# Performance work log

Hardware: AMD Instinct MI355X
Metric: run time of the kernel (lower is better)

## Reference

```python
import jax, jax.numpy as jnp
import numpy as np

B, T, C, H = 4, 1024, 512, 8
HD = C // H
N_NODE, F_DIM, TOTAL_DIM = 64, 8, 16
SCALE = 1.0 / np.sqrt(HD)


def _build_mask():
    # causal tril with every (total_dim-1 mod total_dim)-th COLUMN zeroed
    m = np.tril(np.ones((T, T), dtype=np.float32))
    m[:, TOTAL_DIM - 1::TOTAL_DIM] = 0.0
    return jnp.asarray(m)

MASK = _build_mask()  # (T, T), 1 = keep, 0 = mask


def setup_inputs() -> dict:
    key = jax.random.key(0)
    ks = jax.random.split(key, 12)
    s = 0.02
    return {
        "x": jax.random.normal(ks[0], (B, T, C), dtype=jnp.float32),
        "attn_bias": jax.random.normal(ks[1], (H, N_NODE, N_NODE), dtype=jnp.float32) * 0.1,
        "Wq": jax.random.normal(ks[2], (C, C), dtype=jnp.float32) * s,
        "bq": jax.random.normal(ks[3], (C,), dtype=jnp.float32) * s,
        "Wk": jax.random.normal(ks[4], (C, C), dtype=jnp.float32) * s,
        "bk": jax.random.normal(ks[5], (C,), dtype=jnp.float32) * s,
        "Wv": jax.random.normal(ks[6], (C, C), dtype=jnp.float32) * s,
        "bv": jax.random.normal(ks[7], (C,), dtype=jnp.float32) * s,
        "Wp": jax.random.normal(ks[8], (C, C), dtype=jnp.float32) * s,
        "bp": jax.random.normal(ks[9], (C,), dtype=jnp.float32) * s,
    }


def reference(x, attn_bias, Wq, bq, Wk, bk, Wv, bv, Wp, bp):
    Bx, Tx, Cx = x.shape

    def heads(W, b):  # (B,T,C) -> (B,H,T,HD); torch Linear is x @ W.T + b
        return (x @ W.T + b).reshape(Bx, Tx, H, HD).transpose(0, 2, 1, 3)

    q, k, v = heads(Wq, bq), heads(Wk, bk), heads(Wv, bv)

    # repeat_interleave + repeat expansion == kron(attn_bias, ones(f_dim, f_dim))
    d = N_NODE * F_DIM
    bias = jnp.repeat(jnp.repeat(attn_bias, F_DIM, axis=1), F_DIM, axis=2)  # (H, d, d)
    padded_bias = jnp.zeros((H, Tx, Tx), dtype=x.dtype).at[:, :d, :d].set(bias)

    att = jnp.einsum('bhqd,bhkd->bhqk', q, k) * SCALE + padded_bias[None]
    neg = jnp.asarray(-jnp.inf, dtype=att.dtype)
    att = jnp.where(MASK[None, None, :Tx, :Tx] == 0, neg, att)
    att = jax.nn.softmax(att, axis=-1)

    y = jnp.einsum('bhqk,bhkd->bhqd', att, v)
    y = y.transpose(0, 2, 1, 3).reshape(Bx, Tx, Cx)
    return y @ Wp.T + bp
```

## Files before the change

kernel.cpp:

```cpp
#include <hip/hip_runtime.h>

#define T_SEQ 1024
#define C_DIM 512
#define H_HEADS 8
#define HDIM 64
#define B_BATCH 4
#define M_ROWS (B_BATCH * T_SEQ)
#define NSPLIT_TOT 40

typedef __attribute__((ext_vector_type(8))) short short8;
typedef __attribute__((ext_vector_type(4))) float f32x4;

__device__ __forceinline__ unsigned short f2bf(float f) {
    unsigned u = __builtin_bit_cast(unsigned, f);
    u += 0x7FFFu + ((u >> 16) & 1u);
    return (unsigned short)(u >> 16);
}

__device__ __forceinline__ float bf2f(unsigned short u) {
    return __builtin_bit_cast(float, (unsigned)u << 16);
}

__device__ __forceinline__ void gload_lds16(const unsigned short* g, unsigned short* l) {
    __builtin_amdgcn_global_load_lds(
        (const __attribute__((address_space(1))) unsigned int*)(const void*)g,
        (__attribute__((address_space(3))) unsigned int*)(void*)l, 16, 0, 0);
}

__device__ __constant__ unsigned char BX_OF[NSPLIT_TOT] =
    {0,1,2,3,4,4,5,5,6,6,7,7,8,8,8,9,9,9,10,10,10,11,11,11,
     12,12,12,12,13,13,13,13,14,14,14,14,15,15,15,15};
__device__ __constant__ unsigned char SP_OF[NSPLIT_TOT] =
    {0,0,0,0,0,1,0,1,0,1,0,1,0,1,2,0,1,2,0,1,2,0,1,2,
     0,1,2,3,0,1,2,3,0,1,2,3,0,1,2,3};
__device__ __constant__ unsigned char CUM_OF[16] =
    {0,1,2,3,4,6,8,10,12,15,18,21,24,28,32,36};

__global__ __launch_bounds__(256) void cast_all(
    const float* __restrict__ x,
    const float* __restrict__ wq, const float* __restrict__ wk,
    const float* __restrict__ wv, const float* __restrict__ wp,
    unsigned short* __restrict__ xb,
    unsigned short* __restrict__ wqb, unsigned short* __restrict__ wkb,
    unsigned short* __restrict__ wvb, unsigned short* __restrict__ wpb)
{
    const long NX = (long)M_ROWS * C_DIM;
    const long NW = (long)C_DIM * C_DIM;
    long i4 = (long)blockIdx.x * blockDim.x + threadIdx.x;
    long base = i4 * 4;
    const float* src; unsigned short* dst; long off;
    if (base < NX) { src = x; dst = xb; off = base; }
    else {
        long r = base - NX;
        int w = (int)(r >> 18);
        off = r & (NW - 1);
        switch (w) {
            case 0:  src = wq; dst = wqb; break;
            case 1:  src = wk; dst = wkb; break;
            case 2:  src = wv; dst = wvb; break;
            default: src = wp; dst = wpb; break;
        }
    }
    float4 v = *(const float4*)(src + off);
    ushort4 o;
    o.x = f2bf(v.x); o.y = f2bf(v.y); o.z = f2bf(v.z); o.w = f2bf(v.w);
    *(ushort4*)(dst + off) = o;
}

__device__ __forceinline__ void gemm_body(
    const unsigned short* __restrict__ A,
    const unsigned short* __restrict__ W,
    const float* __restrict__ bias,
    unsigned short* __restrict__ Obf,
    float* __restrict__ Of,
    int mode)
{
    __shared__ __align__(16) unsigned short Atile[128 * 64];
    __shared__ __align__(16) unsigned short Btile[64 * 64];

    const int tid  = threadIdx.x;
    const int w    = tid >> 6;
    const int lane = tid & 63;
    const int quad = lane >> 4;
    const int l16  = lane & 15;
    const int m0   = blockIdx.x * 128;
    const int n0   = blockIdx.y * 64;

    f32x4 acc[2][4] = {};

    const int lr = lane >> 3;
    const int lc = lane & 7;

    for (int k0 = 0; k0 < 512; k0 += 64) {
        __syncthreads();
        for (int i = 0; i < 4; ++i) {
            int r0 = 32 * w + 8 * i;
            int r  = r0 + lr;
            int c  = lc ^ (r & 7);
            gload_lds16(&A[(long)(m0 + r) * 512 + k0 + c * 8], &Atile[r0 * 64]);
        }
        for (int i = 0; i < 2; ++i) {
            int r0 = 16 * w + 8 * i;
            int r  = r0 + lr;
            int c  = lc ^ (r & 7);
            gload_lds16(&W[(long)(n0 + r) * 512 + k0 + c * 8], &Btile[r0 * 64]);
        }
        __syncthreads();

        for (int st = 0; st < 2; ++st) {
            const int pc = ((4 * st + quad) ^ (l16 & 7)) * 8;
            short8 af[2], bf[4];
            for (int i = 0; i < 2; ++i)
                af[i] = *(const short8*)&Atile[(32 * w + 16 * i + l16) * 64 + pc];
            for (int j = 0; j < 4; ++j)
                bf[j] = *(const short8*)&Btile[(16 * j + l16) * 64 + pc];
            for (int i = 0; i < 2; ++i)
                for (int j = 0; j < 4; ++j)
                    acc[i][j] = (mode == 1)
                        ? __builtin_amdgcn_mfma_f32_16x16x32_bf16(bf[j], af[i], acc[i][j], 0, 0, 0)
                        : __builtin_amdgcn_mfma_f32_16x16x32_bf16(af[i], bf[j], acc[i][j], 0, 0, 0);
        }
    }

    if (mode == 1) {
        for (int j = 0; j < 4; ++j) {
            for (int reg = 0; reg < 4; ++reg) {
                int n = n0 + 16 * j + 4 * quad + reg;
                int h = n >> 6, hd = n & 63;
                float bv = bias[n];
                for (int i = 0; i < 2; ++i) {
                    int t = m0 + 32 * w + 16 * i + l16;
                    int b = t >> 10, tl = t & 1023;
                    Obf[(((long)(b * H_HEADS + h)) * HDIM + hd) * T_SEQ + tl] =
                        f2bf(acc[i][j][reg] + bv);
                }
            }
        }
    } else {
        for (int j = 0; j < 4; ++j) {
            int col = n0 + 16 * j + l16;
            float bv = bias[col];
            for (int i = 0; i < 2; ++i) {
                for (int reg = 0; reg < 4; ++reg) {
                    int row = m0 + 32 * w + 16 * i + 4 * quad + reg;
                    float v = acc[i][j][reg] + bv;
                    if (mode == 2) {
                        Of[(long)row * 512 + col] = v;
                    } else {
                        int b = row >> 10, t = row & 1023;
                        int h = col >> 6,  hd = col & 63;
                        Obf[(((long)(b * H_HEADS + h)) * T_SEQ + t) * HDIM + hd] = f2bf(v);
                    }
                }
            }
        }
    }
}

__global__ __launch_bounds__(256) void gemm_qkv(
    const unsigned short* __restrict__ A,
    const unsigned short* __restrict__ Wq, const unsigned short* __restrict__ Wk,
    const unsigned short* __restrict__ Wv,
    const float* __restrict__ bq, const float* __restrict__ bk, const float* __restrict__ bv,
    unsigned short* __restrict__ Q, unsigned short* __restrict__ K,
    unsigned short* __restrict__ V)
{
    const unsigned short* W; const float* b; unsigned short* O; int mode;
    if (blockIdx.z == 0)      { W = Wq; b = bq; O = Q; mode = 0; }
    else if (blockIdx.z == 1) { W = Wk; b = bk; O = K; mode = 0; }
    else                      { W = Wv; b = bv; O = V; mode = 1; }
    gemm_body(A, W, b, O, nullptr, mode);
}

__global__ __launch_bounds__(256) void gemm_out_k(
    const unsigned short* __restrict__ A, const unsigned short* __restrict__ W,
    const float* __restrict__ bias, float* __restrict__ O)
{
    gemm_body(A, W, bias, nullptr, O, 2);
}

__global__ __launch_bounds__(256) void attn_split(
    const unsigned short* __restrict__ Q, const unsigned short* __restrict__ K,
    const unsigned short* __restrict__ Vt, const float* __restrict__ attn_bias,
    unsigned short* __restrict__ Opart, float* __restrict__ lpart)
{
    __shared__ __align__(16) unsigned short Kl[64 * 64];
    __shared__ __align__(16) unsigned short Vl[64 * 64];
    __shared__ __align__(16) unsigned short Pl[4][16 * 72];
    __shared__ float biasl[8][64];

    const int tid  = threadIdx.x;
    const int w    = tid >> 6;
    const int lane = tid & 63;
    const int quad = lane >> 4;
    const int l16  = lane & 15;
    const int lr   = lane >> 3;
    const int lc   = lane & 7;
    const int sidx = blockIdx.x;
    const int bh   = blockIdx.y;
    const int h    = bh & 7;
    const int bx   = BX_OF[sidx];
    const int sp   = SP_OF[sidx];
    const int q0   = bx * 64;
    const int kt0  = sp * 4;
    const int kt1  = min(kt0 + 4, bx + 1);
    const bool use_bias = (q0 < 512) && (sp < 2);
    const int brow = 2 * w + (quad >> 1);
    const int bcol0 = l16 >> 3;

    if (use_bias) {
        for (int i = tid; i < 512; i += 256) {
            int nq = (q0 >> 3) + (i >> 6);
            biasl[i >> 6][i & 63] = attn_bias[h * 4096 + nq * 64 + (i & 63)];
        }
    }

    const unsigned short* Qbh = Q  + (long)bh * T_SEQ * HDIM;
    const unsigned short* Kbh = K  + (long)bh * T_SEQ * HDIM;
    const unsigned short* Vbh = Vt + (long)bh * HDIM * T_SEQ;

    short8 qf[2];
    {
        int qr = q0 + 16 * w + l16;
        qf[0] = *(const short8*)&Qbh[(long)qr * HDIM + 8 * quad];
        qf[1] = *(const short8*)&Qbh[(long)qr * HDIM + 32 + 8 * quad];
    }

    f32x4 oacc[4] = {};
    float lrow[4] = {0.f, 0.f, 0.f, 0.f};
    const int qrb = q0 + 16 * w + 4 * quad;
    const bool colkeep = (l16 != 15);

    for (int kt = kt0; kt < kt1; ++kt) {
        const int k0 = kt * 64;
        __syncthreads();
        for (int i = 0; i < 2; ++i) {
            int r0 = 16 * w + 8 * i;
            int r  = r0 + lr;
            int c  = lc ^ (r & 7);
            gload_lds16(&Kbh[(long)(k0 + r) * HDIM + c * 8], &Kl[r0 * 64]);
            gload_lds16(&Vbh[(long)r * T_SEQ + k0 + c * 8], &Vl[r0 * 64]);
        }
        __syncthreads();

        f32x4 s[4] = {};
        for (int st = 0; st < 2; ++st) {
            const int pc = ((4 * st + quad) ^ (l16 & 7)) * 8;
            for (int ct = 0; ct < 4; ++ct) {
                short8 bf = *(const short8*)&Kl[(16 * ct + l16) * 64 + pc];
                s[ct] = __builtin_amdgcn_mfma_f32_16x16x32_bf16(qf[st], bf, s[ct], 0, 0, 0);
            }
        }

        const bool diag = (kt == bx);
        for (int ct = 0; ct < 4; ++ct) {
            int kcol = k0 + 16 * ct + l16;
            float bval = use_bias ? biasl[brow][(k0 >> 3) + 2 * ct + bcol0] : 0.f;
            for (int reg = 0; reg < 4; ++reg) {
                float v = s[ct][reg] * 0.125f + bval;
                bool keep = colkeep && (!diag || (kcol <= qrb + reg));
                float p = keep ? __expf(v) : 0.f;
                lrow[reg] += p;
                Pl[w][(4 * quad + reg) * 72 + 16 * ct + l16] = f2bf(p);
            }
        }

        for (int st = 0; st < 2; ++st) {
            const int pc = ((4 * st + quad) ^ (l16 & 7)) * 8;
            short8 af = *(const short8*)&Pl[w][l16 * 72 + 32 * st + 8 * quad];
            for (int ct = 0; ct < 4; ++ct) {
                short8 bf = *(const short8*)&Vl[(16 * ct + l16) * 64 + pc];
                oacc[ct] = __builtin_amdgcn_mfma_f32_16x16x32_bf16(af, bf, oacc[ct], 0, 0, 0);
            }
        }
    }

    for (int off = 1; off < 16; off <<= 1)
        for (int reg = 0; reg < 4; ++reg)
            lrow[reg] += __shfl_xor(lrow[reg], off);

    const long p = (long)bh * NSPLIT_TOT + sidx;
    unsigned short* Op = Opart + p * 4096;
    for (int ct = 0; ct < 4; ++ct)
        for (int reg = 0; reg < 4; ++reg)
            Op[(16 * w + 4 * quad + reg) * 64 + 16 * ct + l16] = f2bf(oacc[ct][reg]);
    if (l16 == 0) {
        for (int reg = 0; reg < 4; ++reg) {
            int qr = 16 * w + 4 * quad + reg;
            lpart[p * 64 + qr] = lrow[reg];
        }
    }
}

__global__ __launch_bounds__(256) void attn_combine(
    const unsigned short* __restrict__ Opart, const float* __restrict__ lpart,
    unsigned short* __restrict__ Y)
{
    const int bx = blockIdx.x, bh = blockIdx.y;
    const int b = bh >> 3, h = bh & 7;
    const int ns = (bx >> 2) + 1;
    const long p0 = (long)bh * NSPLIT_TOT + CUM_OF[bx];
    const int tid = threadIdx.x;
    const int qr = tid >> 2;
    const int hs = (tid & 3) * 16;

    float L = 0.f;
    for (int s = 0; s < ns; ++s) L += lpart[(p0 + s) * 64 + qr];

    float acc[16] = {};
    for (int s = 0; s < ns; ++s) {
        const unsigned short* op = Opart + (p0 + s) * 4096 + qr * 64 + hs;
        short8 v0 = *(const short8*)op;
        short8 v1 = *(const short8*)(op + 8);
        for (int k = 0; k < 8; ++k) {
            acc[k]     += bf2f((unsigned short)v0[k]);
            acc[k + 8] += bf2f((unsigned short)v1[k]);
        }
    }
    float inv = 1.f / L;
    int q = bx * 64 + qr;
    unsigned short* y = Y + ((long)b * T_SEQ + q) * C_DIM + h * HDIM + hs;
    for (int j4 = 0; j4 < 4; ++j4) {
        ushort4 o;
        o.x = f2bf(acc[4 * j4 + 0] * inv); o.y = f2bf(acc[4 * j4 + 1] * inv);
        o.z = f2bf(acc[4 * j4 + 2] * inv); o.w = f2bf(acc[4 * j4 + 3] * inv);
        *(ushort4*)(y + 4 * j4) = o;
    }
}

extern "C" void kernel_launch(void* const* d_in, const int* in_sizes, int n_in,
                              void* d_out, int out_size, void* d_ws, size_t ws_size,
                              hipStream_t stream)
{
    const float* x         = (const float*)d_in[0];
    const float* attn_bias = (const float*)d_in[1];
    const float* Wq = (const float*)d_in[2]; const float* bq = (const float*)d_in[3];
    const float* Wk = (const float*)d_in[4]; const float* bk = (const float*)d_in[5];
    const float* Wv = (const float*)d_in[6]; const float* bv = (const float*)d_in[7];
    const float* Wp = (const float*)d_in[8]; const float* bp = (const float*)d_in[9];
    float* out = (float*)d_out;

    const long NX = (long)M_ROWS * C_DIM;
    const long NW = (long)C_DIM * C_DIM;

    unsigned short* xb  = (unsigned short*)d_ws;
    unsigned short* wqb = xb  + NX;
    unsigned short* wkb = wqb + NW;
    unsigned short* wvb = wkb + NW;
    unsigned short* wpb = wvb + NW;
    unsigned short* Qb  = wpb + NW;
    unsigned short* Kb  = Qb  + NX;
    unsigned short* Vtb = Kb  + NX;
    unsigned short* Yb  = Vtb + NX;
    unsigned short* Opart = Yb + NX;
    float* lpart = (float*)(Opart + (long)32 * NSPLIT_TOT * 4096);

    long n4 = (NX + 4 * NW) / 4;
    cast_all<<<dim3((unsigned)(n4 / 256)), 256, 0, stream>>>(
        x, Wq, Wk, Wv, Wp, xb, wqb, wkb, wvb, wpb);

    gemm_qkv<<<dim3(M_ROWS / 128, C_DIM / 64, 3), 256, 0, stream>>>(
        xb, wqb, wkb, wvb, bq, bk, bv, Qb, Kb, Vtb);

    attn_split<<<dim3(NSPLIT_TOT, B_BATCH * H_HEADS), 256, 0, stream>>>(
        Qb, Kb, Vtb, attn_bias, Opart, lpart);

    attn_combine<<<dim3(T_SEQ / 64, B_BATCH * H_HEADS), 256, 0, stream>>>(
        Opart, lpart, Yb);

    gemm_out_k<<<dim3(M_ROWS / 128, C_DIM / 64), 256, 0, stream>>>(
        Yb, wpb, bp, out);
}
```

Baseline: 126.5 us.

## Fuse split-KV combine into attention kernel using last-block atomic counters

```diff
diff --git a/kernel.cpp b/kernel.cpp
--- a/kernel.cpp
+++ b/kernel.cpp
@@ -42,8 +42,13 @@
     const float* __restrict__ wv, const float* __restrict__ wp,
     unsigned short* __restrict__ xb,
     unsigned short* __restrict__ wqb, unsigned short* __restrict__ wkb,
-    unsigned short* __restrict__ wvb, unsigned short* __restrict__ wpb)
-{
+    unsigned short* __restrict__ wvb, unsigned short* __restrict__ wpb,
+    int* __restrict__ counters)
+{
+    if (blockIdx.x == 0) {
+        counters[threadIdx.x] = 0;
+        counters[256 + threadIdx.x] = 0;
+    }
     const long NX = (long)M_ROWS * C_DIM;
     const long NW = (long)C_DIM * C_DIM;
     long i4 = (long)blockIdx.x * blockDim.x + threadIdx.x;
@@ -182,12 +187,14 @@
 __global__ __launch_bounds__(256) void attn_split(
     const unsigned short* __restrict__ Q, const unsigned short* __restrict__ K,
     const unsigned short* __restrict__ Vt, const float* __restrict__ attn_bias,
-    unsigned short* __restrict__ Opart, float* __restrict__ lpart)
+    unsigned short* __restrict__ Opart, float* __restrict__ lpart,
+    int* __restrict__ counters, unsigned short* __restrict__ Y)
 {
     __shared__ __align__(16) unsigned short Kl[64 * 64];
     __shared__ __align__(16) unsigned short Vl[64 * 64];
     __shared__ __align__(16) unsigned short Pl[4][16 * 72];
     __shared__ float biasl[8][64];
+    __shared__ int lastflag;
 
     const int tid  = threadIdx.x;
     const int w    = tid >> 6;
@@ -204,6 +211,7 @@
     const int q0   = bx * 64;
     const int kt0  = sp * 4;
     const int kt1  = min(kt0 + 4, bx + 1);
+    const int ns   = (bx >> 2) + 1;
     const bool use_bias = (q0 < 512) && (sp < 2);
     const int brow = 2 * w + (quad >> 1);
     const int bcol0 = l16 >> 3;
@@ -279,6 +287,19 @@
         for (int reg = 0; reg < 4; ++reg)
             lrow[reg] += __shfl_xor(lrow[reg], off);
 
+    const int b = bh >> 3;
+
+    if (ns == 1) {
+        for (int reg = 0; reg < 4; ++reg) {
+            int qrow = qrb + reg;
+            float inv = 1.f / lrow[reg];
+            unsigned short* y = Y + ((long)b * T_SEQ + qrow) * C_DIM + h * HDIM;
+            for (int ct = 0; ct < 4; ++ct)
+                y[16 * ct + l16] = f2bf(oacc[ct][reg] * inv);
+        }
+        return;
+    }
+
     const long p = (long)bh * NSPLIT_TOT + sidx;
     unsigned short* Op = Opart + p * 4096;
     for (int ct = 0; ct < 4; ++ct)
@@ -290,41 +311,41 @@
             lpart[p * 64 + qr] = lrow[reg];
         }
     }
-}
-
-__global__ __launch_bounds__(256) void attn_combine(
-    const unsigned short* __restrict__ Opart, const float* __restrict__ lpart,
-    unsigned short* __restrict__ Y)
-{
-    const int bx = blockIdx.x, bh = blockIdx.y;
-    const int b = bh >> 3, h = bh & 7;
-    const int ns = (bx >> 2) + 1;
-    const long p0 = (long)bh * NSPLIT_TOT + CUM_OF[bx];
-    const int tid = threadIdx.x;
-    const int qr = tid >> 2;
-    const int hs = (tid & 3) * 16;
-
-    float L = 0.f;
-    for (int s = 0; s < ns; ++s) L += lpart[(p0 + s) * 64 + qr];
-
-    float acc[16] = {};
-    for (int s = 0; s < ns; ++s) {
-        const unsigned short* op = Opart + (p0 + s) * 4096 + qr * 64 + hs;
-        short8 v0 = *(const short8*)op;
-        short8 v1 = *(const short8*)(op + 8);
-        for (int k = 0; k < 8; ++k) {
-            acc[k]     += bf2f((unsigned short)v0[k]);
-            acc[k + 8] += bf2f((unsigned short)v1[k]);
-        }
-    }
-    float inv = 1.f / L;
-    int q = bx * 64 + qr;
-    unsigned short* y = Y + ((long)b * T_SEQ + q) * C_DIM + h * HDIM + hs;
-    for (int j4 = 0; j4 < 4; ++j4) {
-        ushort4 o;
-        o.x = f2bf(acc[4 * j4 + 0] * inv); o.y = f2bf(acc[4 * j4 + 1] * inv);
-        o.z = f2bf(acc[4 * j4 + 2] * inv); o.w = f2bf(acc[4 * j4 + 3] * inv);
-        *(ushort4*)(y + 4 * j4) = o;
+    __threadfence();
+    if (tid == 0) {
+        int old = atomicAdd(&counters[bh * 16 + bx], 1);
+        lastflag = (old == ns - 1);
+    }
+    __syncthreads();
+    if (!lastflag) return;
+
+    {
+        const long p0 = (long)bh * NSPLIT_TOT + CUM_OF[bx];
+        const int qr = tid >> 2;
+        const int hs = (tid & 3) * 16;
+
+        float L = 0.f;
+        for (int s = 0; s < ns; ++s) L += lpart[(p0 + s) * 64 + qr];
+
+        float acc[16] = {};
+        for (int s = 0; s < ns; ++s) {
+            const unsigned short* op = Opart + (p0 + s) * 4096 + qr * 64 + hs;
+            short8 v0 = *(const short8*)op;
+            short8 v1 = *(const short8*)(op + 8);
+            for (int k = 0; k < 8; ++k) {
+                acc[k]     += bf2f((unsigned short)v0[k]);
+                acc[k + 8] += bf2f((unsigned short)v1[k]);
+            }
+        }
+        float inv = 1.f / L;
+        int q = q0 + qr;
+        unsigned short* y = Y + ((long)b * T_SEQ + q) * C_DIM + h * HDIM + hs;
+        for (int j4 = 0; j4 < 4; ++j4) {
+            ushort4 o;
+            o.x = f2bf(acc[4 * j4 + 0] * inv); o.y = f2bf(acc[4 * j4 + 1] * inv);
+            o.z = f2bf(acc[4 * j4 + 2] * inv); o.w = f2bf(acc[4 * j4 + 3] * inv);
+            *(ushort4*)(y + 4 * j4) = o;
+        }
     }
 }
 
@@ -354,19 +375,17 @@
     unsigned short* Yb  = Vtb + NX;
     unsigned short* Opart = Yb + NX;
     float* lpart = (float*)(Opart + (long)32 * NSPLIT_TOT * 4096);
+    int* counters = (int*)(lpart + (long)32 * NSPLIT_TOT * 64);
 
     long n4 = (NX + 4 * NW) / 4;
     cast_all<<<dim3((unsigned)(n4 / 256)), 256, 0, stream>>>(
-        x, Wq, Wk, Wv, Wp, xb, wqb, wkb, wvb, wpb);
+        x, Wq, Wk, Wv, Wp, xb, wqb, wkb, wvb, wpb, counters);
 
     gemm_qkv<<<dim3(M_ROWS / 128, C_DIM / 64, 3), 256, 0, stream>>>(
         xb, wqb, wkb, wvb, bq, bk, bv, Qb, Kb, Vtb);
 
     attn_split<<<dim3(NSPLIT_TOT, B_BATCH * H_HEADS), 256, 0, stream>>>(
-        Qb, Kb, Vtb, attn_bias, Opart, lpart);
-
-    attn_combine<<<dim3(T_SEQ / 64, B_BATCH * H_HEADS), 256, 0, stream>>>(
-        Opart, lpart, Yb);
+        Qb, Kb, Vtb, attn_bias, Opart, lpart, counters, Yb);
 
     gemm_out_k<<<dim3(M_ROWS / 128, C_DIM / 64), 256, 0, stream>>>(
         Yb, wpb, bp, out);
```

New measurement: 286.8 us. 127% more time.
